# Kernel tuning notes

Hardware: AMD Instinct MI355X
Metric: run time of the kernel (lower is better)

Reference implementation:

```python
import jax, jax.numpy as jnp
import numpy as np


def setup_inputs() -> dict:
    key = jax.random.key(0)
    k1, k2 = jax.random.split(key)
    z = jax.random.normal(k1, (16, 256, 4096), dtype=jnp.float32)  # (B, z_dim, T)
    embedding = jax.random.normal(k2, (1024, 256), dtype=jnp.float32)  # (z_num, z_dim)
    return {"z": z, "embedding": embedding}


def reference(z, embedding):
    # z: (B, C, T) -> (B, T, C), matching z.transpose(1, 2)
    zt = jnp.transpose(z, (0, 2, 1))
    B, T, C = zt.shape
    z_flat = zt.reshape(-1, C)  # (N, C), N = B*T

    # squared-euclidean distances: ||z||^2 + ||e||^2 - 2 z e^T  -> (N, K)
    distances = (
        jnp.sum(z_flat * z_flat, axis=1, keepdims=True)
        + jnp.sum(embedding * embedding, axis=1)
        - 2.0 * z_flat @ embedding.T
    )
    encoding_idx = jnp.argmin(distances, axis=1)  # (N,)
    z_vq = embedding[encoding_idx].reshape(B, T, C)

    # perplexity of code usage (one-hot scatter -> mean)
    K = embedding.shape[0]
    counts = jnp.zeros((K,), dtype=jnp.float32).at[encoding_idx].add(1.0)
    avg_probs = counts / encoding_idx.shape[0]
    perplexity = jnp.exp(-jnp.sum(avg_probs * jnp.log(avg_probs + 1e-10)))

    # sparsity = cross_entropy(E E^T, arange) = mean(logsumexp(row) - diag)
    logits = embedding @ embedding.T  # (K, K)
    sparsity = jnp.mean(jax.nn.logsumexp(logits, axis=1) - jnp.diag(logits))

    sg = jax.lax.stop_gradient
    z_qut_loss = jnp.sum((z_vq - sg(zt)) ** 2)   # mse_loss reduction='sum'
    z_enc_loss = jnp.sum((sg(z_vq) - zt) ** 2)

    # straight-through estimator
    z_st = zt + sg(z_vq - zt)
    out = jnp.transpose(z_st, (0, 2, 1))  # back to (B, C, T)
    return (out, z_qut_loss, z_enc_loss, perplexity, sparsity)
```

## Files before the change

### kernel.cpp

```cpp
#include <hip/hip_runtime.h>
#include <math.h>

typedef unsigned int u32;
typedef unsigned long long u64;
typedef _Float16 f16x8 __attribute__((ext_vector_type(8)));
typedef _Float16 f16x4 __attribute__((ext_vector_type(4)));
typedef float f32x4 __attribute__((ext_vector_type(4)));
typedef __attribute__((address_space(1))) const char gch;
typedef __attribute__((address_space(3))) char lch;

#define ZD 256
#define KC 1024
#define TT 4096
#define BB 16
#define NROWS (BB*TT)
#define TAU 0.12f
#define FLAGCAP 32768

__device__ __forceinline__ u32 flip32(float s) {
    int i = __float_as_int(s);
    return (u32)(i ^ ((i >> 31) | 0x80000000));
}
__device__ __forceinline__ float unflip32(u32 u) {
    int m = (~(((int)u) >> 31)) | 0x80000000;
    return __int_as_float((int)(u ^ (u32)m));
}

__global__ __launch_bounds__(256)
void vq_prep_kernel(const float* __restrict__ emb, _Float16* __restrict__ eh,
                    float* __restrict__ re, int* __restrict__ cnt) {
    int gid = blockIdx.x * 256 + threadIdx.x;
    if (gid < 2) cnt[gid] = 0;

    int code = gid >> 6;
    int lane = threadIdx.x & 63;
    float4 v = *(const float4*)(emb + (size_t)code * ZD + lane * 4);
    float s = v.x*v.x + v.y*v.y + v.z*v.z + v.w*v.w;
    #pragma unroll
    for (int off = 32; off; off >>= 1) s += __shfl_down(s, off, 64);
    if (lane == 0) re[code] = s;

    f16x4 hv;
    hv[0] = (_Float16)v.x; hv[1] = (_Float16)v.y;
    hv[2] = (_Float16)v.z; hv[3] = (_Float16)v.w;
    *(f16x4*)(eh + (size_t)code * ZD + lane * 4) = hv;
}

__device__ __forceinline__ void stage_half8(const char* ehc, char* dstbase,
                                            int h, int w, int l) {
    const int srow = h * 16384;
    #pragma unroll
    for (int j = 0; j < 2; ++j) {
        const int gi  = w * 2 + j;
        const int c   = 2 * gi + (l >> 5);
        const int kbs = (l & 31) * 16;
        const int off = srow + c * 512 + (kbs ^ ((c & 7) << 4));
        __builtin_amdgcn_global_load_lds((gch*)(ehc + off),
                                         (lch*)(dstbase + gi * 1024), 16, 0, 0);
    }
}

__device__ __forceinline__ void compute_phase16(const char* hb, int h,
                                                const f16x8 (&ah)[8], const float* reL,
                                                float (&v1)[4], float (&v2)[4], int (&i1)[4],
                                                int lane15, int lk) {
    #pragma unroll
    for (int cg = 0; cg < 2; ++cg) {
        const int c  = cg * 16 + lane15;
        const int sw = (lane15 & 7) << 4;
        f16x8 bh[8];
        #pragma unroll
        for (int ks = 0; ks < 8; ++ks)
            bh[ks] = *(const f16x8*)(hb + c * 512 + ((lk * 16 + ks * 64) ^ sw));

        f32x4 ae = {0.f, 0.f, 0.f, 0.f};
        f32x4 ao = {0.f, 0.f, 0.f, 0.f};
        __builtin_amdgcn_s_setprio(1);
        #pragma unroll
        for (int ks = 0; ks < 4; ++ks) {
            ae = __builtin_amdgcn_mfma_f32_16x16x32_f16(ah[2 * ks],     bh[2 * ks],     ae, 0, 0, 0);
            ao = __builtin_amdgcn_mfma_f32_16x16x32_f16(ah[2 * ks + 1], bh[2 * ks + 1], ao, 0, 0, 0);
        }
        __builtin_amdgcn_s_setprio(0);

        const int codeg = h * 32 + c;
        const float rc = reL[codeg];
        #pragma unroll
        for (int r = 0; r < 4; ++r) {
            float s0 = fmaf(-2.f, ae[r] + ao[r], rc);
            float n2 = fminf(fmaxf(v1[r], s0), v2[r]);
            i1[r] = (s0 < v1[r]) ? codeg : i1[r];
            v1[r] = fminf(v1[r], s0);
            v2[r] = n2;
        }
    }
}

__global__ __launch_bounds__(512, 4)
void vq_argmin_mfma(const float* __restrict__ z, const _Float16* __restrict__ eh,
                    const float* __restrict__ emb, const float* __restrict__ re,
                    float* __restrict__ out, float* __restrict__ lossP,
                    int* __restrict__ idx, int* __restrict__ cnt,
                    int* __restrict__ flags) {
    __shared__ __align__(16) char lds[53248];
    float* reL    = (float*)(lds + 49152);
    int*   idsL   = (int*)lds;
    float* wlossL = (float*)(lds + 1024);

    const int tid = threadIdx.x;
    const int w   = tid >> 6;
    const int l   = tid & 63;
    const int lane15 = l & 15;
    const int lk     = l >> 4;
    const int r0  = blockIdx.x * 128;
    const int b   = r0 >> 12;
    const int t0  = r0 & 4095;
    const char* ehc = (const char*)eh;

    *(float2*)(reL + tid * 2) = *(const float2*)(re + tid * 2);

    f16x8 ah[8];
    float zsq = 0.f;
    {
        const char* zb = (const char*)(z + (size_t)b * ZD * TT + t0 + w * 16);
        char* zdst = lds + w * 4096;
        #pragma unroll
        for (int round = 0; round < 4; ++round) {
            #pragma unroll
            for (int j = 0; j < 4; ++j) {
                const int cl = j * 16 + (l >> 2);
                const int tb = (l & 3) * 16;
                const int c  = round * 64 + cl;
                const char* src = zb + (size_t)c * TT * 4 + tb;
                __builtin_amdgcn_global_load_lds((gch*)src, (lch*)(zdst + j * 1024),
                                                 16, 0, 0);
            }
            asm volatile("s_waitcnt vmcnt(0)" ::: "memory");
            __builtin_amdgcn_sched_barrier(0);
            #pragma unroll
            for (int ks2 = 0; ks2 < 2; ++ks2) {
                const int cl0 = ks2 * 32 + lk * 8;
                f16x8 h;
                #pragma unroll
                for (int j = 0; j < 8; ++j) {
                    float v = *(const float*)(zdst + (cl0 + j) * 64 + lane15 * 4);
                    zsq = fmaf(v, v, zsq);
                    h[j] = (_Float16)v;
                }
                ah[round * 2 + ks2] = h;
            }
            asm volatile("s_waitcnt lgkmcnt(0)" ::: "memory");
            __builtin_amdgcn_sched_barrier(0);
        }
    }
    zsq += __shfl_xor(zsq, 16, 64);
    zsq += __shfl_xor(zsq, 32, 64);

    float v1[4], v2[4];
    int   i1[4];
    #pragma unroll
    for (int r = 0; r < 4; ++r) { v1[r] = 3.4e38f; v2[r] = 3.4e38f; i1[r] = 0; }

    asm volatile("s_waitcnt vmcnt(0) lgkmcnt(0)" ::: "memory");
    __syncthreads();
    stage_half8(ehc, lds,         0, w, l);
    stage_half8(ehc, lds + 16384, 1, w, l);

    for (int h = 0; h < 31; ++h) {
        asm volatile("s_waitcnt vmcnt(2)" ::: "memory");
        __builtin_amdgcn_sched_barrier(0);
        __builtin_amdgcn_s_barrier();
        if (h < 30) stage_half8(ehc, lds + ((h + 2) % 3) * 16384, h + 2, w, l);
        compute_phase16(lds + (h % 3) * 16384, h, ah, reL, v1, v2, i1, lane15, lk);
    }
    asm volatile("s_waitcnt vmcnt(0)" ::: "memory");
    __builtin_amdgcn_sched_barrier(0);
    __builtin_amdgcn_s_barrier();
    compute_phase16(lds + (31 % 3) * 16384, 31, ah, reL, v1, v2, i1, lane15, lk);

    #pragma unroll
    for (int off = 1; off < 16; off <<= 1) {
        #pragma unroll
        for (int r = 0; r < 4; ++r) {
            float ov1 = __shfl_xor(v1[r], off, 64);
            int   oi1 = __shfl_xor(i1[r], off, 64);
            float ov2 = __shfl_xor(v2[r], off, 64);
            float nv2 = fminf(fmaxf(v1[r], ov1), fminf(v2[r], ov2));
            if (ov1 < v1[r] || (ov1 == v1[r] && oi1 < i1[r])) { v1[r] = ov1; i1[r] = oi1; }
            v2[r] = nv2;
        }
    }

    float zsr[4];
    #pragma unroll
    for (int r = 0; r < 4; ++r) zsr[r] = __shfl(zsq, lk * 4 + r, 64);

    __syncthreads();
    float lossw = 0.f;
    if (lane15 == 0) {
        #pragma unroll
        for (int r = 0; r < 4; ++r) {
            const int row = w * 16 + lk * 4 + r;
            idsL[row] = i1[r];
            const bool fl = (v2[r] - v1[r] < TAU);
            lossw += fl ? zsr[r] : (zsr[r] + v1[r]);
            if (fl) {
                int p = atomicAdd(cnt, 1);
                if (p < FLAGCAP) flags[p] = (r0 + row) | (i1[r] << 16);
            }
        }
    }
    lossw += __shfl_xor(lossw, 16, 64);
    lossw += __shfl_xor(lossw, 32, 64);
    if (l == 0) wlossL[w] = lossw;
    __syncthreads();

    if (tid < 128) idx[r0 + tid] = idsL[tid];
    if (tid == 0) {
        float s = 0.f;
        #pragma unroll
        for (int j = 0; j < 8; ++j) s += wlossL[j];
        lossP[blockIdx.x] = s;
    }

    {
        const int c0 = w * 32;
        float* ob = out + (size_t)b * ZD * TT + t0;
        #pragma unroll
        for (int half = 0; half < 2; ++half) {
            const int tt = half * 64 + l;
            const int ii = idsL[tt];
            const float4* er4 = (const float4*)(emb + (size_t)ii * ZD + c0);
            #pragma unroll
            for (int c4 = 0; c4 < 8; ++c4) {
                float4 ev = er4[c4];
                float* o0 = ob + (size_t)(c0 + c4 * 4) * TT + tt;
                o0[0]      = ev.x;
                o0[TT]     = ev.y;
                o0[2 * TT] = ev.z;
                o0[3 * TT] = ev.w;
            }
        }
    }
}

__global__ __launch_bounds__(256)
void vq_fixup_spar(const float* __restrict__ z, const float* __restrict__ emb,
                   const float* __restrict__ re, const int* __restrict__ cnt,
                   const int* __restrict__ flags, float* __restrict__ out,
                   int* __restrict__ idx, float* __restrict__ sparM,
                   float* __restrict__ sparS, float* __restrict__ addP) {
    const int tid = threadIdx.x;
    const int w   = tid >> 6;
    const int lane = tid & 63;

    if (blockIdx.x >= 256) {
        __shared__ __align__(16) float er[8][260];
        __shared__ float wmaxS[8][4];
        __shared__ float wsumS[8][4];
        const int sb = blockIdx.x - 256;
        const int r0 = (sb >> 2) * 8;
        const int ch = sb & 3;
        const int c  = ch * 256 + tid;

        for (int i = tid; i < 8 * 256; i += 256) er[i >> 8][i & 255] = emb[(size_t)r0 * ZD + i];
        __syncthreads();

        const float4* ec = (const float4*)(emb + (size_t)c * ZD);
        float a[8] = {0.f,0.f,0.f,0.f,0.f,0.f,0.f,0.f};
        #pragma unroll 4
        for (int k4 = 0; k4 < ZD / 4; ++k4) {
            float4 e4 = ec[k4];
            #pragma unroll
            for (int r = 0; r < 8; ++r) {
                const float* a4 = &er[r][k4 * 4];
                a[r] = fmaf(e4.x, a4[0], fmaf(e4.y, a4[1],
                       fmaf(e4.z, a4[2], fmaf(e4.w, a4[3], a[r]))));
            }
        }
        #pragma unroll
        for (int r = 0; r < 8; ++r) {
            float m = a[r];
            #pragma unroll
            for (int off = 32; off; off >>= 1) m = fmaxf(m, __shfl_xor(m, off, 64));
            if (lane == 0) wmaxS[r][w] = m;
        }
        __syncthreads();
        #pragma unroll
        for (int r = 0; r < 8; ++r) {
            const float M = fmaxf(fmaxf(wmaxS[r][0], wmaxS[r][1]),
                                  fmaxf(wmaxS[r][2], wmaxS[r][3]));
            float se = expf(a[r] - M);
            #pragma unroll
            for (int off = 32; off; off >>= 1) se += __shfl_xor(se, off, 64);
            if (lane == 0) wsumS[r][w] = se;
        }
        __syncthreads();
        if (tid < 8) {
            const float M = fmaxf(fmaxf(wmaxS[tid][0], wmaxS[tid][1]),
                                  fmaxf(wmaxS[tid][2], wmaxS[tid][3]));
            const float S = wsumS[tid][0] + wsumS[tid][1]
                          + wsumS[tid][2] + wsumS[tid][3];
            sparM[ch * KC + r0 + tid] = M;
            sparS[ch * KC + r0 + tid] = S;
        }
        return;
    }

    __shared__ __align__(16) float zs[8][ZD];
    __shared__ u64 sb2[4][8];
    __shared__ int nwS[8];
    __shared__ float addS;
    int n = cnt[0];
    if (n > FLAGCAP) n = FLAGCAP;
    float blkLoss = 0.f;

    for (int base = blockIdx.x * 8; base < n; base += 256 * 8) {
        const int nr = (n - base < 8) ? (n - base) : 8;
        __syncthreads();
        for (int i = tid; i < nr * 256; i += 256) {
            const int r = i >> 8, k = i & 255;
            const int rowg = flags[base + r] & 0xFFFF;
            zs[r][k] = z[(size_t)(rowg >> 12) * ZD * TT + (size_t)k * TT + (rowg & 4095)];
        }
        __syncthreads();

        u64 best[8];
        #pragma unroll
        for (int r = 0; r < 8; ++r) best[r] = 0xFFFFFFFFFFFFFFFFull;

        for (int cc = 0; cc < 4; ++cc) {
            const int c = cc * 256 + tid;
            const float4* ec = (const float4*)(emb + (size_t)c * ZD);
            float a[8] = {0.f,0.f,0.f,0.f,0.f,0.f,0.f,0.f};
            #pragma unroll 4
            for (int k4 = 0; k4 < ZD / 4; ++k4) {
                float4 e4 = ec[k4];
                #pragma unroll
                for (int r = 0; r < 8; ++r) {
                    const float* a4 = &zs[r][k4 * 4];
                    a[r] = fmaf(e4.x, a4[0], fmaf(e4.y, a4[1],
                           fmaf(e4.z, a4[2], fmaf(e4.w, a4[3], a[r]))));
                }
            }
            const float rc = re[c];
            #pragma unroll
            for (int r = 0; r < 8; ++r) {
                if (r < nr) {
                    float s = fmaf(-2.f, a[r], rc);
                    u64 pk = ((u64)flip32(s) << 32) | (u32)c;
                    if (pk < best[r]) best[r] = pk;
                }
            }
        }
        #pragma unroll
        for (int r = 0; r < 8; ++r) {
            if (r < nr) {
                u64 bv = best[r];
                #pragma unroll
                for (int off = 32; off; off >>= 1) {
                    u64 o = (u64)__shfl_xor((long long)bv, off, 64);
                    if (o < bv) bv = o;
                }
                if (lane == 0) sb2[w][r] = bv;
            }
        }
        __syncthreads();
        if (tid == 0) addS = 0.f;
        __syncthreads();
        if (tid < nr) {
            u64 m = sb2[0][tid];
            if (sb2[1][tid] < m) m = sb2[1][tid];
            if (sb2[2][tid] < m) m = sb2[2][tid];
            if (sb2[3][tid] < m) m = sb2[3][tid];
            const int nc  = (int)(u32)(m & 0xFFFFFFFFull);
            const float s = unflip32((u32)(m >> 32));
            const int rowg = flags[base + tid] & 0xFFFF;
            const int old  = (flags[base + tid] >> 16) & 1023;
            atomicAdd(&addS, s);
            if (nc != old) { idx[rowg] = nc; nwS[tid] = nc; }
            else nwS[tid] = -1;
        }
        __syncthreads();
        if (tid == 0) blkLoss += addS;
        for (int r = 0; r < nr; ++r) {
            const int nw = nwS[r];
            if (nw >= 0) {
                const int rowg = flags[base + r] & 0xFFFF;
                out[(size_t)(rowg >> 12) * ZD * TT + (size_t)tid * TT + (rowg & 4095)]
                    = emb[(size_t)nw * ZD + tid];
            }
        }
    }
    if (tid == 0) addP[blockIdx.x] = blkLoss;
}

__global__ __launch_bounds__(1024)
void vq_final_kernel(const int* __restrict__ idx, const float* __restrict__ re,
                     const float* __restrict__ sparM, const float* __restrict__ sparS,
                     const float* __restrict__ lossP, const float* __restrict__ addP,
                     float* __restrict__ scal) {
    __shared__ int   histL[4][1024];
    __shared__ float red[1024];
    const int tid = threadIdx.x;
    const int g   = tid >> 8;

    histL[0][tid] = 0; histL[1][tid] = 0; histL[2][tid] = 0; histL[3][tid] = 0;
    __syncthreads();
    #pragma unroll 4
    for (int i = 0; i < 64; ++i)
        atomicAdd(&histL[g][idx[i * 1024 + tid]], 1);
    __syncthreads();
    const int hc = histL[0][tid] + histL[1][tid] + histL[2][tid] + histL[3][tid];
    float p = (float)hc * (1.0f / (float)NROWS);
    red[tid] = -p * logf(p + 1e-10f);
    __syncthreads();
    for (int st = 512; st; st >>= 1) {
        if (tid < st) red[tid] += red[tid + st];
        __syncthreads();
    }
    if (tid == 0) scal[2] = expf(red[0]);
    __syncthreads();

    red[tid] = (tid < 512 ? lossP[tid] : 0.f) + ((tid < 256) ? addP[tid] : 0.f);
    __syncthreads();
    for (int st = 512; st; st >>= 1) {
        if (tid < st) red[tid] += red[tid + st];
        __syncthreads();
    }
    if (tid == 0) { scal[0] = red[0]; scal[1] = red[0]; }
    __syncthreads();

    {
        const float m0 = sparM[tid], m1 = sparM[KC + tid];
        const float m2 = sparM[2 * KC + tid], m3 = sparM[3 * KC + tid];
        const float M = fmaxf(fmaxf(m0, m1), fmaxf(m2, m3));
        const float S = sparS[tid] * expf(m0 - M) + sparS[KC + tid] * expf(m1 - M)
                      + sparS[2 * KC + tid] * expf(m2 - M) + sparS[3 * KC + tid] * expf(m3 - M);
        red[tid] = M + logf(S) - re[tid];
    }
    __syncthreads();
    for (int st = 512; st; st >>= 1) {
        if (tid < st) red[tid] += red[tid + st];
        __syncthreads();
    }
    if (tid == 0) scal[3] = red[0] * (1.0f / (float)KC);
}

extern "C" void kernel_launch(void* const* d_in, const int* in_sizes, int n_in,
                              void* d_out, int out_size, void* d_ws, size_t ws_size,
                              hipStream_t stream) {
    const float* z   = (const float*)d_in[0];
    const float* emb = (const float*)d_in[1];
    float* out = (float*)d_out;
    const size_t NOUT = (size_t)BB * ZD * TT;
    float* scal = out + NOUT;

    float* re    = (float*)d_ws;
    int*   cnt   = (int*)(re + KC);
    int*   flags = cnt + 4;
    float* sparM = (float*)(flags + FLAGCAP);
    float* sparS = sparM + 4 * KC;
    float* lossP = sparS + 4 * KC;
    float* addP  = lossP + 512;
    int*   idx   = (int*)(addP + 256);
    _Float16* eh = (_Float16*)(idx + NROWS);

    vq_prep_kernel<<<256, 256, 0, stream>>>(emb, eh, re, cnt);
    vq_argmin_mfma<<<NROWS / 128, 512, 0, stream>>>(z, eh, emb, re, out, lossP, idx,
                                                    cnt, flags);
    vq_fixup_spar<<<768, 256, 0, stream>>>(z, emb, re, cnt, flags, out, idx,
                                           sparM, sparS, addP);
    vq_final_kernel<<<1, 1024, 0, stream>>>(idx, re, sparM, sparS, lossP, addP, scal);
}
```

Measured before the change: 177.6 us.

## Split fixup and sparsity kernels; widen fixup blocks to cover all codes at once

```diff
diff --git a/kernel.cpp b/kernel.cpp
--- a/kernel.cpp
+++ b/kernel.cpp
@@ -244,135 +244,67 @@
     }
 }
 
-__global__ __launch_bounds__(256)
-void vq_fixup_spar(const float* __restrict__ z, const float* __restrict__ emb,
-                   const float* __restrict__ re, const int* __restrict__ cnt,
-                   const int* __restrict__ flags, float* __restrict__ out,
-                   int* __restrict__ idx, float* __restrict__ sparM,
-                   float* __restrict__ sparS, float* __restrict__ addP) {
+__global__ __launch_bounds__(1024)
+void vq_fixup_kernel(const float* __restrict__ z, const float* __restrict__ emb,
+                     const float* __restrict__ re, const int* __restrict__ cnt,
+                     const int* __restrict__ flags, float* __restrict__ out,
+                     int* __restrict__ idx, float* __restrict__ addP) {
+    __shared__ __align__(16) float zs[8][ZD];
+    __shared__ u64 sb[16][8];
+    __shared__ int nwS[8];
+    __shared__ float addS;
     const int tid = threadIdx.x;
     const int w   = tid >> 6;
     const int lane = tid & 63;
-
-    if (blockIdx.x >= 256) {
-        __shared__ __align__(16) float er[8][260];
-        __shared__ float wmaxS[8][4];
-        __shared__ float wsumS[8][4];
-        const int sb = blockIdx.x - 256;
-        const int r0 = (sb >> 2) * 8;
-        const int ch = sb & 3;
-        const int c  = ch * 256 + tid;
-
-        for (int i = tid; i < 8 * 256; i += 256) er[i >> 8][i & 255] = emb[(size_t)r0 * ZD + i];
-        __syncthreads();
-
-        const float4* ec = (const float4*)(emb + (size_t)c * ZD);
+    int n = cnt[0];
+    if (n > FLAGCAP) n = FLAGCAP;
+    float blkLoss = 0.f;
+
+    const int c = tid;
+    const float4* ec = (const float4*)(emb + (size_t)c * ZD);
+    const float rc = re[c];
+
+    for (int base = blockIdx.x * 8; base < n; base += 256 * 8) {
+        const int nr = (n - base < 8) ? (n - base) : 8;
+        __syncthreads();
+        for (int i = tid; i < nr * 256; i += 1024) {
+            const int r = i >> 8, k = i & 255;
+            const int rowg = flags[base + r] & 0xFFFF;
+            zs[r][k] = z[(size_t)(rowg >> 12) * ZD * TT + (size_t)k * TT + (rowg & 4095)];
+        }
+        __syncthreads();
+
         float a[8] = {0.f,0.f,0.f,0.f,0.f,0.f,0.f,0.f};
         #pragma unroll 4
         for (int k4 = 0; k4 < ZD / 4; ++k4) {
             float4 e4 = ec[k4];
             #pragma unroll
             for (int r = 0; r < 8; ++r) {
-                const float* a4 = &er[r][k4 * 4];
+                const float* a4 = &zs[r][k4 * 4];
                 a[r] = fmaf(e4.x, a4[0], fmaf(e4.y, a4[1],
                        fmaf(e4.z, a4[2], fmaf(e4.w, a4[3], a[r]))));
             }
         }
         #pragma unroll
         for (int r = 0; r < 8; ++r) {
-            float m = a[r];
-            #pragma unroll
-            for (int off = 32; off; off >>= 1) m = fmaxf(m, __shfl_xor(m, off, 64));
-            if (lane == 0) wmaxS[r][w] = m;
-        }
-        __syncthreads();
-        #pragma unroll
-        for (int r = 0; r < 8; ++r) {
-            const float M = fmaxf(fmaxf(wmaxS[r][0], wmaxS[r][1]),
-                                  fmaxf(wmaxS[r][2], wmaxS[r][3]));
-            float se = expf(a[r] - M);
-            #pragma unroll
-            for (int off = 32; off; off >>= 1) se += __shfl_xor(se, off, 64);
-            if (lane == 0) wsumS[r][w] = se;
-        }
-        __syncthreads();
-        if (tid < 8) {
-            const float M = fmaxf(fmaxf(wmaxS[tid][0], wmaxS[tid][1]),
-                                  fmaxf(wmaxS[tid][2], wmaxS[tid][3]));
-            const float S = wsumS[tid][0] + wsumS[tid][1]
-                          + wsumS[tid][2] + wsumS[tid][3];
-            sparM[ch * KC + r0 + tid] = M;
-            sparS[ch * KC + r0 + tid] = S;
-        }
-        return;
-    }
-
-    __shared__ __align__(16) float zs[8][ZD];
-    __shared__ u64 sb2[4][8];
-    __shared__ int nwS[8];
-    __shared__ float addS;
-    int n = cnt[0];
-    if (n > FLAGCAP) n = FLAGCAP;
-    float blkLoss = 0.f;
-
-    for (int base = blockIdx.x * 8; base < n; base += 256 * 8) {
-        const int nr = (n - base < 8) ? (n - base) : 8;
-        __syncthreads();
-        for (int i = tid; i < nr * 256; i += 256) {
-            const int r = i >> 8, k = i & 255;
-            const int rowg = flags[base + r] & 0xFFFF;
-            zs[r][k] = z[(size_t)(rowg >> 12) * ZD * TT + (size_t)k * TT + (rowg & 4095)];
-        }
-        __syncthreads();
-
-        u64 best[8];
-        #pragma unroll
-        for (int r = 0; r < 8; ++r) best[r] = 0xFFFFFFFFFFFFFFFFull;
-
-        for (int cc = 0; cc < 4; ++cc) {
-            const int c = cc * 256 + tid;
-            const float4* ec = (const float4*)(emb + (size_t)c * ZD);
-            float a[8] = {0.f,0.f,0.f,0.f,0.f,0.f,0.f,0.f};
-            #pragma unroll 4
-            for (int k4 = 0; k4 < ZD / 4; ++k4) {
-                float4 e4 = ec[k4];
-                #pragma unroll
-                for (int r = 0; r < 8; ++r) {
-                    const float* a4 = &zs[r][k4 * 4];
-                    a[r] = fmaf(e4.x, a4[0], fmaf(e4.y, a4[1],
-                           fmaf(e4.z, a4[2], fmaf(e4.w, a4[3], a[r]))));
-                }
-            }
-            const float rc = re[c];
-            #pragma unroll
-            for (int r = 0; r < 8; ++r) {
-                if (r < nr) {
-                    float s = fmaf(-2.f, a[r], rc);
-                    u64 pk = ((u64)flip32(s) << 32) | (u32)c;
-                    if (pk < best[r]) best[r] = pk;
-                }
-            }
-        }
-        #pragma unroll
-        for (int r = 0; r < 8; ++r) {
             if (r < nr) {
-                u64 bv = best[r];
+                float s = fmaf(-2.f, a[r], rc);
+                u64 bv = ((u64)flip32(s) << 32) | (u32)c;
                 #pragma unroll
                 for (int off = 32; off; off >>= 1) {
                     u64 o = (u64)__shfl_xor((long long)bv, off, 64);
                     if (o < bv) bv = o;
                 }
-                if (lane == 0) sb2[w][r] = bv;
+                if (lane == 0) sb[w][r] = bv;
             }
         }
         __syncthreads();
         if (tid == 0) addS = 0.f;
         __syncthreads();
         if (tid < nr) {
-            u64 m = sb2[0][tid];
-            if (sb2[1][tid] < m) m = sb2[1][tid];
-            if (sb2[2][tid] < m) m = sb2[2][tid];
-            if (sb2[3][tid] < m) m = sb2[3][tid];
+            u64 m = sb[0][tid];
+            #pragma unroll
+            for (int j = 1; j < 16; ++j) if (sb[j][tid] < m) m = sb[j][tid];
             const int nc  = (int)(u32)(m & 0xFFFFFFFFull);
             const float s = unflip32((u32)(m >> 32));
             const int rowg = flags[base + tid] & 0xFFFF;
@@ -385,7 +317,7 @@
         if (tid == 0) blkLoss += addS;
         for (int r = 0; r < nr; ++r) {
             const int nw = nwS[r];
-            if (nw >= 0) {
+            if (nw >= 0 && tid < 256) {
                 const int rowg = flags[base + r] & 0xFFFF;
                 out[(size_t)(rowg >> 12) * ZD * TT + (size_t)tid * TT + (rowg & 4095)]
                     = emb[(size_t)nw * ZD + tid];
@@ -393,6 +325,63 @@
         }
     }
     if (tid == 0) addP[blockIdx.x] = blkLoss;
+}
+
+__global__ __launch_bounds__(256)
+void vq_spar_kernel(const float* __restrict__ emb, float* __restrict__ sparM,
+                    float* __restrict__ sparS) {
+    __shared__ __align__(16) float er[8][260];
+    __shared__ float wmaxS[8][4];
+    __shared__ float wsumS[8][4];
+    const int tid = threadIdx.x;
+    const int w   = tid >> 6;
+    const int lane = tid & 63;
+    const int sb = blockIdx.x;
+    const int r0 = (sb >> 2) * 8;
+    const int ch = sb & 3;
+    const int c  = ch * 256 + tid;
+
+    for (int i = tid; i < 8 * 256; i += 256) er[i >> 8][i & 255] = emb[(size_t)r0 * ZD + i];
+    __syncthreads();
+
+    const float4* ec = (const float4*)(emb + (size_t)c * ZD);
+    float a[8] = {0.f,0.f,0.f,0.f,0.f,0.f,0.f,0.f};
+    #pragma unroll 4
+    for (int k4 = 0; k4 < ZD / 4; ++k4) {
+        float4 e4 = ec[k4];
+        #pragma unroll
+        for (int r = 0; r < 8; ++r) {
+            const float* a4 = &er[r][k4 * 4];
+            a[r] = fmaf(e4.x, a4[0], fmaf(e4.y, a4[1],
+                   fmaf(e4.z, a4[2], fmaf(e4.w, a4[3], a[r]))));
+        }
+    }
+    #pragma unroll
+    for (int r = 0; r < 8; ++r) {
+        float m = a[r];
+        #pragma unroll
+        for (int off = 32; off; off >>= 1) m = fmaxf(m, __shfl_xor(m, off, 64));
+        if (lane == 0) wmaxS[r][w] = m;
+    }
+    __syncthreads();
+    #pragma unroll
+    for (int r = 0; r < 8; ++r) {
+        const float M = fmaxf(fmaxf(wmaxS[r][0], wmaxS[r][1]),
+                              fmaxf(wmaxS[r][2], wmaxS[r][3]));
+        float se = expf(a[r] - M);
+        #pragma unroll
+        for (int off = 32; off; off >>= 1) se += __shfl_xor(se, off, 64);
+        if (lane == 0) wsumS[r][w] = se;
+    }
+    __syncthreads();
+    if (tid < 8) {
+        const float M = fmaxf(fmaxf(wmaxS[tid][0], wmaxS[tid][1]),
+                              fmaxf(wmaxS[tid][2], wmaxS[tid][3]));
+        const float S = wsumS[tid][0] + wsumS[tid][1]
+                      + wsumS[tid][2] + wsumS[tid][3];
+        sparM[ch * KC + r0 + tid] = M;
+        sparS[ch * KC + r0 + tid] = S;
+    }
 }
 
 __global__ __launch_bounds__(1024)
@@ -469,7 +458,7 @@
     vq_prep_kernel<<<256, 256, 0, stream>>>(emb, eh, re, cnt);
     vq_argmin_mfma<<<NROWS / 128, 512, 0, stream>>>(z, eh, emb, re, out, lossP, idx,
                                                     cnt, flags);
-    vq_fixup_spar<<<768, 256, 0, stream>>>(z, emb, re, cnt, flags, out, idx,
-                                           sparM, sparS, addP);
+    vq_spar_kernel<<<512, 256, 0, stream>>>(emb, sparM, sparS);
+    vq_fixup_kernel<<<256, 1024, 0, stream>>>(z, emb, re, cnt, flags, out, idx, addP);
     vq_final_kernel<<<1, 1024, 0, stream>>>(idx, re, sparM, sparS, lossP, addP, scal);
 }
```

Result: faster. 163.0 us (-8.2%).
